# Kernel optimization log

Hardware: AMD Instinct MI355X
Metric: run time of the kernel (lower is better)

## Reference

```python
import jax, jax.numpy as jnp
import numpy as np

B, N = 32, 1024


def setup_inputs() -> dict:
    key = jax.random.key(0)
    return {"SSMap": jax.random.normal(key, (B, N, N), dtype=jnp.float32)}


def reference(SSMap):
    # Faithful vectorization of Loss_Reg:
    #   for each sample, for each super-diagonal d = 1..N-1, diag_d = {x[i, i+d]},
    #   len(diag_d) = N - d. Loss uses d = 1..N-2 (the last, length-1 diagonal is
    #   skipped, which also avoids torch.std's NaN on a single element):
    #     std(diag_d * (N-d) / 20)  ==  ((N-d)/20) * std_unbiased(diag_d)
    #   then mean over diagonals, then mean over batch.
    Bn, Nn, _ = SSMap.shape
    ii, jj = jnp.triu_indices(Nn, k=1)          # strict upper triangle, M = N(N-1)/2
    seg = jj - ii - 1                            # diagonal id in [0, N-2]; diag d -> seg d-1
    nseg = Nn - 1

    vals = SSMap[:, ii, jj]                      # [B, M] gather of all super-diagonals

    seg_sum = jax.vmap(lambda v: jax.ops.segment_sum(v, seg, num_segments=nseg))(vals)
    seg_sq = jax.vmap(lambda v: jax.ops.segment_sum(v * v, seg, num_segments=nseg))(vals)

    cnt = (Nn - 1 - jnp.arange(nseg)).astype(SSMap.dtype)   # [nseg], count of diag d = N-d
    mean = seg_sum / cnt
    # unbiased variance (torch.std default, ddof=1)
    var = (seg_sq - cnt * mean * mean) / (cnt - 1.0)
    std_scaled = jnp.sqrt(jnp.maximum(var, 0.0)) * cnt / 20.0   # [B, nseg]

    # original excludes the last diagonal (length 1)
    per_sample = jnp.mean(std_scaled[:, : nseg - 1], axis=1)    # [B]
    return jnp.mean(per_sample)
```

## Files before the change

### kernel.cpp

```cpp
#include <hip/hip_runtime.h>
#include <hip/hip_bf16.h>

#define BATCH 32
#define NDIM  1024
#define NSEGP 1024
#define NUSE  1022
#define BLK   256
#define G     64
#define ROWS  16
#define RBLK  64

typedef float f4a __attribute__((ext_vector_type(4), aligned(4)));
typedef float f4  __attribute__((ext_vector_type(4), aligned(16)));

__global__ __launch_bounds__(BLK) void seg_partial_kernel(
        const float* __restrict__ S,
        float* __restrict__ part)
{
    const int b  = blockIdx.x >> 6;
    const int g  = blockIdx.x & (G - 1);
    const int c0 = threadIdx.x << 2;

    float s0 = 0.f, s1 = 0.f, s2 = 0.f, s3 = 0.f;
    float q0 = 0.f, q1 = 0.f, q2 = 0.f, q3 = 0.f;

    const float* p = S + (size_t)b * NDIM * NDIM + (size_t)g * (NDIM + 1) + 1 + c0;

    #pragma unroll
    for (int m = 0; m < ROWS; ++m) {
        const int i = g + (m << 6);
        if (i < NDIM - 1) {
            const int rem = NDIM - 1 - i;
            if (c0 < rem) {
                f4a v = __builtin_nontemporal_load((const f4a*)p);
                float v0 = v.x;
                float v1 = (c0 + 1 < rem) ? v.y : 0.f;
                float v2 = (c0 + 2 < rem) ? v.z : 0.f;
                float v3 = (c0 + 3 < rem) ? v.w : 0.f;
                s0 += v0; q0 += v0 * v0;
                s1 += v1; q1 += v1 * v1;
                s2 += v2; q2 += v2 * v2;
                s3 += v3; q3 += v3 * v3;
            }
        }
        p += 64 * NDIM + 64;
    }

    float* psum = part + (size_t)blockIdx.x * (2 * NSEGP);
    ((f4*)psum)[threadIdx.x]           = (f4){s0, s1, s2, s3};
    ((f4*)(psum + NSEGP))[threadIdx.x] = (f4){q0, q1, q2, q3};
}

__global__ __launch_bounds__(RBLK) void reduce_kernel(
        const float* __restrict__ part,
        float* __restrict__ cpart)
{
    const int b  = blockIdx.x >> 2;
    const int c  = blockIdx.x & 3;
    const int t  = threadIdx.x;
    const int s0 = (c << 8) + (t << 2);
    const int qi = s0 >> 2;

    f4 sum = {0.f, 0.f, 0.f, 0.f};
    f4 sq  = {0.f, 0.f, 0.f, 0.f};
    const float* p = part + (size_t)b * G * (2 * NSEGP);
    #pragma unroll
    for (int g = 0; g < G; ++g) {
        f4 a = ((const f4*)(p + (size_t)g * (2 * NSEGP)))[qi];
        f4 z = ((const f4*)(p + (size_t)g * (2 * NSEGP) + NSEGP))[qi];
        sum += a;
        sq  += z;
    }

    float acc = 0.f;
    #pragma unroll
    for (int r = 0; r < 4; ++r) {
        const int s = s0 + r;
        if (s < NUSE) {
            float cnt  = (float)(NDIM - 1 - s);
            float mean = sum[r] / cnt;
            float var  = (sq[r] - cnt * mean * mean) / (cnt - 1.0f);
            acc += sqrtf(fmaxf(var, 0.0f)) * cnt * 0.05f;
        }
    }

    #pragma unroll
    for (int off = 32; off > 0; off >>= 1)
        acc += __shfl_down(acc, off, 64);
    if (t == 0) cpart[blockIdx.x] = acc;
}

__global__ void final_kernel(const float* __restrict__ cpart,
                             float* __restrict__ out)
{
    float v = cpart[threadIdx.x] + cpart[threadIdx.x + 64];
    #pragma unroll
    for (int off = 32; off > 0; off >>= 1)
        v += __shfl_down(v, off, 64);
    if (threadIdx.x == 0)
        out[0] = v / (float)(BATCH * NUSE);
}

extern "C" void kernel_launch(void* const* d_in, const int* in_sizes, int n_in,
                              void* d_out, int out_size, void* d_ws, size_t ws_size,
                              hipStream_t stream) {
    const float* S = (const float*)d_in[0];
    float* out = (float*)d_out;

    float* part  = (float*)d_ws;
    float* cpart = part + (size_t)BATCH * G * 2 * NSEGP;

    seg_partial_kernel<<<BATCH * G, BLK, 0, stream>>>(S, part);
    reduce_kernel<<<BATCH * 4, RBLK, 0, stream>>>(part, cpart);
    final_kernel<<<1, 64, 0, stream>>>(cpart, out);
}
```

Baseline: 183.8 us.

## Align diagonal loads to 16 bytes and widen reduce kernel parallelism

The partial kernel shifts each row's load pointer back to a 16-byte boundary so vector loads are aligned, masks the out-of-range lanes, and realigns the partial sums through shared memory before storing. The reduce kernel now uses 256-thread blocks and 8 chunks per batch, splitting the 64 group partials across warps and combining them in LDS, which gives many more threads for the second pass. The cost is extra LDS traffic, barriers and masking in the first kernel.

```diff
diff --git a/kernel.cpp b/kernel.cpp
--- a/kernel.cpp
+++ b/kernel.cpp
@@ -1,5 +1,4 @@
 #include <hip/hip_runtime.h>
-#include <hip/hip_bf16.h>
 
 #define BATCH 32
 #define NDIM  1024
@@ -8,10 +7,10 @@
 #define BLK   256
 #define G     64
 #define ROWS  16
-#define RBLK  64
+#define RB    256
+#define CHUNKS 8
 
-typedef float f4a __attribute__((ext_vector_type(4), aligned(4)));
-typedef float f4  __attribute__((ext_vector_type(4), aligned(16)));
+typedef float f4 __attribute__((ext_vector_type(4), aligned(16)));
 
 __global__ __launch_bounds__(BLK) void seg_partial_kernel(
         const float* __restrict__ S,
@@ -19,81 +18,114 @@
 {
     const int b  = blockIdx.x >> 6;
     const int g  = blockIdx.x & (G - 1);
+    const int r  = (g + 1) & 3;
     const int c0 = threadIdx.x << 2;
 
     float s0 = 0.f, s1 = 0.f, s2 = 0.f, s3 = 0.f;
     float q0 = 0.f, q1 = 0.f, q2 = 0.f, q3 = 0.f;
 
-    const float* p = S + (size_t)b * NDIM * NDIM + (size_t)g * (NDIM + 1) + 1 + c0;
+    const float* p = S + (size_t)b * NDIM * NDIM + (size_t)g * (NDIM + 1) + 1 - r + c0;
 
     #pragma unroll
     for (int m = 0; m < ROWS; ++m) {
         const int i = g + (m << 6);
         if (i < NDIM - 1) {
-            const int rem = NDIM - 1 - i;
-            if (c0 < rem) {
-                f4a v = __builtin_nontemporal_load((const f4a*)p);
-                float v0 = v.x;
-                float v1 = (c0 + 1 < rem) ? v.y : 0.f;
-                float v2 = (c0 + 2 < rem) ? v.z : 0.f;
-                float v3 = (c0 + 3 < rem) ? v.w : 0.f;
+            const int hi = NDIM - 2 - i + r;
+            if (c0 <= hi) {
+                f4 v = __builtin_nontemporal_load((const f4*)p);
+                float v0 = (c0 + 0 >= r && c0 + 0 <= hi) ? v.x : 0.f;
+                float v1 = (c0 + 1 >= r && c0 + 1 <= hi) ? v.y : 0.f;
+                float v2 = (c0 + 2 >= r && c0 + 2 <= hi) ? v.z : 0.f;
+                float v3 = (c0 + 3 <= hi) ? v.w : 0.f;
                 s0 += v0; q0 += v0 * v0;
                 s1 += v1; q1 += v1 * v1;
                 s2 += v2; q2 += v2 * v2;
                 s3 += v3; q3 += v3 * v3;
             }
         }
-        p += 64 * NDIM + 64;
+        p += (size_t)64 * (NDIM + 1);
     }
 
+    __shared__ float lds[NSEGP + 4];
+    if (threadIdx.x < 4) lds[NSEGP + threadIdx.x] = 0.f;
+
     float* psum = part + (size_t)blockIdx.x * (2 * NSEGP);
-    ((f4*)psum)[threadIdx.x]           = (f4){s0, s1, s2, s3};
-    ((f4*)(psum + NSEGP))[threadIdx.x] = (f4){q0, q1, q2, q3};
+
+    lds[c0 + 0] = s0; lds[c0 + 1] = s1; lds[c0 + 2] = s2; lds[c0 + 3] = s3;
+    __syncthreads();
+    f4 o;
+    o.x = lds[c0 + r + 0]; o.y = lds[c0 + r + 1];
+    o.z = lds[c0 + r + 2]; o.w = lds[c0 + r + 3];
+    ((f4*)psum)[threadIdx.x] = o;
+    __syncthreads();
+
+    lds[c0 + 0] = q0; lds[c0 + 1] = q1; lds[c0 + 2] = q2; lds[c0 + 3] = q3;
+    __syncthreads();
+    o.x = lds[c0 + r + 0]; o.y = lds[c0 + r + 1];
+    o.z = lds[c0 + r + 2]; o.w = lds[c0 + r + 3];
+    ((f4*)(psum + NSEGP))[threadIdx.x] = o;
 }
 
-__global__ __launch_bounds__(RBLK) void reduce_kernel(
+__global__ __launch_bounds__(RB) void reduce_kernel(
         const float* __restrict__ part,
         float* __restrict__ cpart)
 {
-    const int b  = blockIdx.x >> 2;
-    const int c  = blockIdx.x & 3;
+    const int b  = blockIdx.x >> 3;
+    const int c  = blockIdx.x & (CHUNKS - 1);
     const int t  = threadIdx.x;
-    const int s0 = (c << 8) + (t << 2);
-    const int qi = s0 >> 2;
+    const int q  = t & 31;
+    const int gs = t >> 5;
+    const int qi = (c << 5) + q;
 
     f4 sum = {0.f, 0.f, 0.f, 0.f};
     f4 sq  = {0.f, 0.f, 0.f, 0.f};
     const float* p = part + (size_t)b * G * (2 * NSEGP);
     #pragma unroll
-    for (int g = 0; g < G; ++g) {
-        f4 a = ((const f4*)(p + (size_t)g * (2 * NSEGP)))[qi];
-        f4 z = ((const f4*)(p + (size_t)g * (2 * NSEGP) + NSEGP))[qi];
-        sum += a;
-        sq  += z;
+    for (int k = 0; k < 8; ++k) {
+        const int g = (gs << 3) + k;
+        const f4* pg = (const f4*)(p + (size_t)g * (2 * NSEGP));
+        sum += pg[qi];
+        sq  += pg[(NSEGP >> 2) + qi];
     }
 
-    float acc = 0.f;
-    #pragma unroll
-    for (int r = 0; r < 4; ++r) {
-        const int s = s0 + r;
-        if (s < NUSE) {
-            float cnt  = (float)(NDIM - 1 - s);
-            float mean = sum[r] / cnt;
-            float var  = (sq[r] - cnt * mean * mean) / (cnt - 1.0f);
-            acc += sqrtf(fmaxf(var, 0.0f)) * cnt * 0.05f;
+    __shared__ f4 lsum[8][32];
+    __shared__ f4 lsq [8][32];
+    lsum[gs][q] = sum;
+    lsq [gs][q] = sq;
+    __syncthreads();
+
+    if (t < 64) {
+        float acc = 0.f;
+        if (t < 32) {
+            f4 S = {0.f, 0.f, 0.f, 0.f};
+            f4 Q = {0.f, 0.f, 0.f, 0.f};
+            #pragma unroll
+            for (int k = 0; k < 8; ++k) { S += lsum[k][t]; Q += lsq[k][t]; }
+            #pragma unroll
+            for (int rr = 0; rr < 4; ++rr) {
+                const int s = (c << 7) + (t << 2) + rr;
+                if (s < NUSE) {
+                    float cnt  = (float)(NDIM - 1 - s);
+                    float mean = S[rr] / cnt;
+                    float var  = (Q[rr] - cnt * mean * mean) / (cnt - 1.0f);
+                    acc += sqrtf(fmaxf(var, 0.0f)) * cnt * 0.05f;
+                }
+            }
         }
+        #pragma unroll
+        for (int off = 32; off > 0; off >>= 1)
+            acc += __shfl_down(acc, off, 64);
+        if (t == 0) cpart[blockIdx.x] = acc;
     }
-
-    #pragma unroll
-    for (int off = 32; off > 0; off >>= 1)
-        acc += __shfl_down(acc, off, 64);
-    if (t == 0) cpart[blockIdx.x] = acc;
 }
 
 __global__ void final_kernel(const float* __restrict__ cpart,
                              float* __restrict__ out)
 {
-    float v = cpart[threadIdx.x] + cpart[threadIdx.x + 64];
+    float v = 0.f;
+    #pragma unroll
+    for (int k = 0; k < 4; ++k)
+        v += cpart[threadIdx.x + (k << 6)];
     #pragma unroll
     for (int off = 32; off > 0; off >>= 1)
         v += __shfl_down(v, off, 64);
@@ -111,6 +143,6 @@
     float* cpart = part + (size_t)BATCH * G * 2 * NSEGP;
 
     seg_partial_kernel<<<BATCH * G, BLK, 0, stream>>>(S, part);
-    reduce_kernel<<<BATCH * 4, RBLK, 0, stream>>>(part, cpart);
+    reduce_kernel<<<BATCH * CHUNKS, RB, 0, stream>>>(part, cpart);
     final_kernel<<<1, 64, 0, stream>>>(cpart, out);
 }
```

After: 178.9 us. 2.7% less time.
